# Optimization experiments

Measured on AMD Instinct MI355X. Metric: run time of the kernel, lower is better.

Reference implementation:

```python
import jax, jax.numpy as jnp
import numpy as np

D_MODEL = 1024
NUM_HEADS = 16
D_HEAD = D_MODEL // NUM_HEADS
THETA = 10000.0
B, S = 2, 2048


def setup_inputs() -> dict:
    key = jax.random.key(0)
    ks = jax.random.split(key, 5)
    std = np.sqrt(2.0 / (D_MODEL + D_MODEL))
    x = jax.random.normal(ks[0], (B, S, D_MODEL), dtype=jnp.float32)
    Wq = jax.random.normal(ks[1], (D_MODEL, D_MODEL), dtype=jnp.float32) * std
    Wk = jax.random.normal(ks[2], (D_MODEL, D_MODEL), dtype=jnp.float32) * std
    Wv = jax.random.normal(ks[3], (D_MODEL, D_MODEL), dtype=jnp.float32) * std
    Wo = jax.random.normal(ks[4], (D_MODEL, D_MODEL), dtype=jnp.float32) * std
    token_positions = jnp.arange(S, dtype=jnp.int32)
    return {"x": x, "Wq": Wq, "Wk": Wk, "Wv": Wv, "Wo": Wo,
            "token_positions": token_positions}


def _apply_rope(t, token_positions):
    # t: [B, H, S, d_head]; interleaved (even/odd) RoPE
    dh = t.shape[-1]
    inv_freq = 1.0 / (THETA ** (jnp.arange(0, dh, 2, dtype=jnp.float32) / dh))
    freqs = token_positions.astype(jnp.float32)[:, None] * inv_freq  # [S, dh/2]
    cos = jnp.cos(freqs)  # broadcasts over B, H
    sin = jnp.sin(freqs)
    x1 = t[..., 0::2]
    x2 = t[..., 1::2]
    r1 = x1 * cos - x2 * sin
    r2 = x1 * sin + x2 * cos
    return jnp.stack([r1, r2], axis=-1).reshape(t.shape)


def reference(x, Wq, Wk, Wv, Wo, token_positions):
    b, s, d = x.shape
    h, dh = NUM_HEADS, D_HEAD

    def proj(W):
        y = x @ W.T  # [B, S, D]
        return y.reshape(b, s, h, dh).transpose(0, 2, 1, 3)  # [B, H, S, dh]

    q = _apply_rope(proj(Wq), token_positions)
    k = _apply_rope(proj(Wk), token_positions)
    v = proj(Wv)

    scores = jnp.einsum('bhqd,bhkd->bhqk', q, k) / jnp.sqrt(jnp.float32(dh))
    causal = jnp.tril(jnp.ones((s, s), dtype=bool))
    scores = jnp.where(causal, scores, jnp.float32(-jnp.inf))
    attn = jax.nn.softmax(scores, axis=-1)
    out = jnp.einsum('bhqk,bhkd->bhqd', attn, v)  # [B, H, S, dh]
    out = out.transpose(0, 2, 1, 3).reshape(b, s, d)
    return out @ Wo.T
```

## Files before the change

### kernel.cpp

```cpp
#include <hip/hip_runtime.h>
#include <hip/hip_bf16.h>
#include <math.h>

#define DMODEL 1024
#define NHEAD  16
#define DHEAD  64
#define BATCH  2
#define SEQ    2048
#define MROWS  (BATCH * SEQ)

typedef __attribute__((ext_vector_type(8))) __bf16 bf16x8;
typedef __attribute__((ext_vector_type(4))) float  f32x4;

__device__ __forceinline__ void load16_lds(const ushort* g, ushort* l) {
    __builtin_amdgcn_global_load_lds(
        (const __attribute__((address_space(1))) unsigned int*)g,
        (__attribute__((address_space(3))) unsigned int*)l, 16, 0, 0);
}

__device__ __forceinline__ ushort bf16u(float v) {
    __hip_bfloat16 h = __float2bfloat16(v);
    return *reinterpret_cast<ushort*>(&h);
}

__global__ __launch_bounds__(256)
void cast_f32_bf16(const float* __restrict__ s, ushort* __restrict__ d, int n) {
    const int i = (blockIdx.x * 256 + threadIdx.x) * 8;
    if (i >= n) return;
    const f32x4 a = *reinterpret_cast<const f32x4*>(s + i);
    const f32x4 b = *reinterpret_cast<const f32x4*>(s + i + 4);
    bf16x8 o;
    #pragma unroll
    for (int j = 0; j < 4; j++) { o[j] = (__bf16)a[j]; o[4 + j] = (__bf16)b[j]; }
    *reinterpret_cast<bf16x8*>(d + i) = o;
}

__global__ __launch_bounds__(256)
void cast_w4(const float* __restrict__ w0, const float* __restrict__ w1,
             const float* __restrict__ w2, const float* __restrict__ w3,
             ushort* __restrict__ dst) {
    const float* src = (blockIdx.y == 0) ? w0 : (blockIdx.y == 1) ? w1
                     : (blockIdx.y == 2) ? w2 : w3;
    const int i = (blockIdx.x * 256 + threadIdx.x) * 8;
    const f32x4 a = *reinterpret_cast<const f32x4*>(src + i);
    const f32x4 b = *reinterpret_cast<const f32x4*>(src + i + 4);
    bf16x8 o;
    #pragma unroll
    for (int j = 0; j < 4; j++) { o[j] = (__bf16)a[j]; o[4 + j] = (__bf16)b[j]; }
    *reinterpret_cast<bf16x8*>(dst + (size_t)blockIdx.y * DMODEL * DMODEL + i) = o;
}

__global__ __launch_bounds__(256)
void gemm_qkv(const ushort* __restrict__ A, const ushort* __restrict__ B,
              ushort* __restrict__ C) {
    __shared__ __align__(16) ushort As[128 * 32];
    __shared__ __align__(16) ushort Bs[128 * 32];
    const int tid  = threadIdx.x;
    const int m0   = blockIdx.y * 128;
    const int n0   = blockIdx.x * 128;
    const int lane = tid & 63;
    const int w    = tid >> 6;
    const int l16  = lane & 15;
    const int quad = lane >> 4;
    const int wm   = (w >> 1) * 64;
    const int wn   = (w & 1) * 64;
    const int srow = tid >> 2;
    const int scol = (tid & 3) * 8;

    f32x4 acc[4][4];
    #pragma unroll
    for (int i = 0; i < 4; i++)
        #pragma unroll
        for (int j = 0; j < 4; j++) acc[i][j] = (f32x4){0.f, 0.f, 0.f, 0.f};

    for (int k0 = 0; k0 < DMODEL; k0 += 32) {
        __syncthreads();
        #pragma unroll
        for (int half = 0; half < 2; half++) {
            const int row = srow + half * 64;
            load16_lds(A + (size_t)(m0 + row) * DMODEL + k0 + scol,
                       &As[row * 32 + scol]);
            load16_lds(B + (size_t)(n0 + row) * DMODEL + k0 + scol,
                       &Bs[row * 32 + scol]);
        }
        __syncthreads();
        bf16x8 af[4], bfr[4];
        #pragma unroll
        for (int s = 0; s < 4; s++)
            af[s] = *reinterpret_cast<const bf16x8*>(
                &As[(wm + s * 16 + l16) * 32 + quad * 8]);
        #pragma unroll
        for (int s = 0; s < 4; s++)
            bfr[s] = *reinterpret_cast<const bf16x8*>(
                &Bs[(wn + s * 16 + l16) * 32 + quad * 8]);
        #pragma unroll
        for (int i = 0; i < 4; i++)
            #pragma unroll
            for (int j = 0; j < 4; j++)
                acc[i][j] = __builtin_amdgcn_mfma_f32_16x16x32_bf16(
                    af[i], bfr[j], acc[i][j], 0, 0, 0);
    }

    const int nbase  = n0 + wn;
    const int tensor = nbase >> 10;
    const int hh     = (nbase & 1023) >> 6;
    if (tensor < 2) {
        ushort* Dt = C + (size_t)tensor * ((size_t)MROWS * DMODEL);
        #pragma unroll
        for (int i = 0; i < 4; i++)
            #pragma unroll
            for (int r = 0; r < 4; r++) {
                const int m  = m0 + wm + i * 16 + quad * 4 + r;
                const int bb = m >> 11;
                const int ss = m & (SEQ - 1);
                #pragma unroll
                for (int j = 0; j < 4; j++) {
                    const int dh = j * 16 + l16;
                    Dt[(((size_t)(bb * NHEAD + hh)) * SEQ + ss) * DHEAD + dh] =
                        bf16u(acc[i][j][r]);
                }
            }
    } else {
        ushort* Dv = C + 2 * ((size_t)MROWS * DMODEL);
        #pragma unroll
        for (int i = 0; i < 4; i++)
            #pragma unroll
            for (int r = 0; r < 4; r++) {
                const int m = m0 + wm + i * 16 + quad * 4 + r;
                #pragma unroll
                for (int j = 0; j < 4; j++) {
                    const int row = hh * 64 + j * 16 + l16;
                    Dv[(size_t)row * MROWS + m] = bf16u(acc[i][j][r]);
                }
            }
    }
}

__global__ __launch_bounds__(256)
void gemm_out64(const ushort* __restrict__ A, const ushort* __restrict__ B,
                float* __restrict__ C) {
    __shared__ __align__(16) ushort As[64 * 32];
    __shared__ __align__(16) ushort Bs[128 * 32];
    const int tid  = threadIdx.x;
    const int m0   = blockIdx.y * 64;
    const int n0   = blockIdx.x * 128;
    const int lane = tid & 63;
    const int w    = tid >> 6;
    const int l16  = lane & 15;
    const int quad = lane >> 4;
    const int wm   = (w >> 1) * 32;
    const int wn   = (w & 1) * 64;
    const int srow = tid >> 2;
    const int scol = (tid & 3) * 8;

    f32x4 acc[2][4];
    #pragma unroll
    for (int i = 0; i < 2; i++)
        #pragma unroll
        for (int j = 0; j < 4; j++) acc[i][j] = (f32x4){0.f, 0.f, 0.f, 0.f};

    for (int k0 = 0; k0 < DMODEL; k0 += 32) {
        __syncthreads();
        {
            const int m  = m0 + srow;
            const int bb = m >> 11;
            const int ss = m & (SEQ - 1);
            const int kk = k0 + scol;
            const int h  = kk >> 6;
            const int dh = kk & 63;
            load16_lds(A + (((size_t)(bb * NHEAD + h)) * SEQ + ss) * DHEAD + dh,
                       &As[srow * 32 + scol]);
        }
        #pragma unroll
        for (int half = 0; half < 2; half++) {
            const int row = srow + half * 64;
            load16_lds(B + (size_t)(n0 + row) * DMODEL + k0 + scol,
                       &Bs[row * 32 + scol]);
        }
        __syncthreads();
        bf16x8 af[2], bfr[4];
        #pragma unroll
        for (int s = 0; s < 2; s++)
            af[s] = *reinterpret_cast<const bf16x8*>(
                &As[(wm + s * 16 + l16) * 32 + quad * 8]);
        #pragma unroll
        for (int s = 0; s < 4; s++)
            bfr[s] = *reinterpret_cast<const bf16x8*>(
                &Bs[(wn + s * 16 + l16) * 32 + quad * 8]);
        #pragma unroll
        for (int i = 0; i < 2; i++)
            #pragma unroll
            for (int j = 0; j < 4; j++)
                acc[i][j] = __builtin_amdgcn_mfma_f32_16x16x32_bf16(
                    af[i], bfr[j], acc[i][j], 0, 0, 0);
    }
    #pragma unroll
    for (int i = 0; i < 2; i++)
        #pragma unroll
        for (int r = 0; r < 4; r++) {
            const int m = m0 + wm + i * 16 + quad * 4 + r;
            #pragma unroll
            for (int j = 0; j < 4; j++)
                C[(size_t)m * DMODEL + n0 + wn + j * 16 + l16] = acc[i][j][r];
        }
}

__global__ __launch_bounds__(256)
void rope_bf16(__hip_bfloat16* __restrict__ q, __hip_bfloat16* __restrict__ k,
               const int* __restrict__ pos) {
    const int idx = blockIdx.x * blockDim.x + threadIdx.x;
    const int total = BATCH * NHEAD * SEQ * (DHEAD / 2);
    if (idx >= total) return;
    const int i  = idx & 31;
    const int s  = (idx >> 5) & (SEQ - 1);
    const int bh = idx >> 16;
    const float p = (float)pos[s];
    const float freq = p * powf(10000.0f, -(float)(2 * i) / (float)DHEAD);
    float sn, cs;
    sincosf(freq, &sn, &cs);
    const size_t base = (((size_t)bh * SEQ + s) * DHEAD) + 2 * i;
    float x1 = __bfloat162float(q[base]), x2 = __bfloat162float(q[base + 1]);
    q[base]     = __float2bfloat16(x1 * cs - x2 * sn);
    q[base + 1] = __float2bfloat16(x1 * sn + x2 * cs);
    x1 = __bfloat162float(k[base]); x2 = __bfloat162float(k[base + 1]);
    k[base]     = __float2bfloat16(x1 * cs - x2 * sn);
    k[base + 1] = __float2bfloat16(x1 * sn + x2 * cs);
}

__global__ __launch_bounds__(256)
void attn_mfma6(const ushort* __restrict__ qb, const ushort* __restrict__ kb,
                const ushort* __restrict__ vtg, ushort* __restrict__ ob) {
    __shared__ __align__(16) ushort Ks[2][4096];
    __shared__ __align__(16) ushort Vs[2][4096];
    __shared__ ushort Pb[4][16][72];

    const int bh   = blockIdx.x;
    const int b    = bh >> 4;
    const int h    = bh & 15;
    const int qt   = (gridDim.y - 1) - blockIdx.y;
    const int tid  = threadIdx.x;
    const int w    = tid >> 6;
    const int lane = tid & 63;
    const int l16  = lane & 15;
    const int quad = lane >> 4;
    const size_t base = (size_t)bh * SEQ * DHEAD;

    const int qlo = qt * 64 + w * 16;

    const float SC = 0.125f * 1.44269504088896f;
    bf16x8 qa[2];
    {
        const size_t qo = base + (size_t)(qlo + l16) * DHEAD + quad * 8;
        qa[0] = *reinterpret_cast<const bf16x8*>(qb + qo);
        qa[1] = *reinterpret_cast<const bf16x8*>(qb + qo + 32);
        #pragma unroll
        for (int j = 0; j < 8; j++) {
            qa[0][j] = (__bf16)(SC * (float)qa[0][j]);
            qa[1][j] = (__bf16)(SC * (float)qa[1][j]);
        }
    }

    f32x4 oacc[4];
    #pragma unroll
    for (int s = 0; s < 4; s++) oacc[s] = (f32x4){0.f, 0.f, 0.f, 0.f};
    float l_ = 0.f;

    const int c0 = tid,        r0 = c0 >> 3, g0 = (c0 & 7) ^ (r0 & 7);
    const int c1 = 256 + tid,  r1 = c1 >> 3, g1 = (c1 & 7) ^ (r1 & 7);
    const ushort* kg0 = kb + base + (size_t)r0 * DHEAD + g0 * 8;
    const ushort* kg1 = kb + base + (size_t)r1 * DHEAD + g1 * 8;
    const ushort* vg0 = vtg + (size_t)(h * DHEAD + r0) * MROWS + b * SEQ + g0 * 8;
    const ushort* vg1 = vtg + (size_t)(h * DHEAD + r1) * MROWS + b * SEQ + g1 * 8;

    int koff[2][4];
    #pragma unroll
    for (int half = 0; half < 2; half++)
        #pragma unroll
        for (int sub = 0; sub < 4; sub++)
            koff[half][sub] = (sub * 16 + l16) * 64 +
                              (((half * 4 + quad) ^ (l16 & 7)) * 8);

    load16_lds(kg0, &Ks[0][c0 * 8]);
    load16_lds(kg1, &Ks[0][c1 * 8]);
    load16_lds(vg0, &Vs[0][c0 * 8]);
    load16_lds(vg1, &Vs[0][c1 * 8]);

    const int T = qt + 1;
    for (int t = 0; t < T; t++) {
        const int bf = t & 1;
        __syncthreads();
        if (t + 1 < T) {
            const size_t ko = (size_t)(t + 1) * 64 * DHEAD;
            const int    vo = (t + 1) * 64;
            load16_lds(kg0 + ko, &Ks[bf ^ 1][c0 * 8]);
            load16_lds(kg1 + ko, &Ks[bf ^ 1][c1 * 8]);
            load16_lds(vg0 + vo, &Vs[bf ^ 1][c0 * 8]);
            load16_lds(vg1 + vo, &Vs[bf ^ 1][c1 * 8]);
        }

        const bool diag = (t == qt);
        const int nsub = diag ? (w + 1) : 4;
        const int nhv  = diag ? ((w >> 1) + 1) : 2;

        f32x4 sacc[4];
        #pragma unroll
        for (int s = 0; s < 4; s++) sacc[s] = (f32x4){0.f, 0.f, 0.f, 0.f};
        #pragma unroll
        for (int half = 0; half < 2; half++)
            #pragma unroll
            for (int sub = 0; sub < 4; sub++)
                if (sub < nsub) {
                    const bf16x8 kf = *reinterpret_cast<const bf16x8*>(
                        &Ks[bf][koff[half][sub]]);
                    sacc[sub] = __builtin_amdgcn_mfma_f32_16x16x32_bf16(
                        kf, qa[half], sacc[sub], 0, 0, 0);
                }

        float ev[4][4];
        if (diag) {
            const int thr = qlo + l16 - t * 64;
            #pragma unroll
            for (int sub = 0; sub < 4; sub++)
                #pragma unroll
                for (int r = 0; r < 4; r++) {
                    const float e = (sub * 16 + quad * 4 + r <= thr)
                                        ? exp2f(sacc[sub][r]) : 0.f;
                    ev[sub][r] = e;
                    l_ += e;
                }
        } else {
            #pragma unroll
            for (int sub = 0; sub < 4; sub++)
                #pragma unroll
                for (int r = 0; r < 4; r++) {
                    const float e = exp2f(sacc[sub][r]);
                    ev[sub][r] = e;
                    l_ += e;
                }
        }

        #pragma unroll
        for (int sub = 0; sub < 4; sub++) {
            ushort4 pk;
            pk.x = bf16u(ev[sub][0]); pk.y = bf16u(ev[sub][1]);
            pk.z = bf16u(ev[sub][2]); pk.w = bf16u(ev[sub][3]);
            *reinterpret_cast<ushort4*>(&Pb[w][l16][sub * 16 + quad * 4]) = pk;
        }
        bf16x8 pa[2];
        pa[0] = *reinterpret_cast<const bf16x8*>(&Pb[w][l16][quad * 8]);
        pa[1] = *reinterpret_cast<const bf16x8*>(&Pb[w][l16][32 + quad * 8]);

        #pragma unroll
        for (int hk = 0; hk < 2; hk++) {
            if (hk >= nhv) break;
            #pragma unroll
            for (int sf = 0; sf < 4; sf++) {
                const bf16x8 vf = *reinterpret_cast<const bf16x8*>(
                    &Vs[bf][koff[hk][sf]]);
                oacc[sf] = __builtin_amdgcn_mfma_f32_16x16x32_bf16(
                    pa[hk], vf, oacc[sf], 0, 0, 0);
            }
        }
    }

    l_ += __shfl_xor(l_, 16, 64);
    l_ += __shfl_xor(l_, 32, 64);
    float inv[4];
    #pragma unroll
    for (int r = 0; r < 4; r++) inv[r] = 1.f / __shfl(l_, quad * 4 + r, 64);
    #pragma unroll
    for (int sub = 0; sub < 4; sub++)
        #pragma unroll
        for (int r = 0; r < 4; r++) {
            const int q = qlo + quad * 4 + r;
            ob[base + (size_t)q * DHEAD + sub * 16 + l16] =
                bf16u(oacc[sub][r] * inv[r]);
        }
}

extern "C" void kernel_launch(void* const* d_in, const int* in_sizes, int n_in,
                              void* d_out, int out_size, void* d_ws, size_t ws_size,
                              hipStream_t stream) {
    const float* x  = (const float*)d_in[0];
    const float* Wq = (const float*)d_in[1];
    const float* Wk = (const float*)d_in[2];
    const float* Wv = (const float*)d_in[3];
    const float* Wo = (const float*)d_in[4];
    const int* pos = (const int*)d_in[5];

    const size_t TEN = (size_t)MROWS * DMODEL;
    const size_t WEL = (size_t)DMODEL * DMODEL;
    ushort* xb   = (ushort*)d_ws;
    ushort* Wqkv = xb + TEN;
    ushort* Wob  = Wqkv + 3 * WEL;
    ushort* qb   = Wob + WEL;
    ushort* kb   = qb + TEN;
    ushort* vtb  = kb + TEN;
    ushort* ob   = vtb + TEN;

    dim3 blk(256);
    cast_f32_bf16<<<TEN / (8 * 256), blk, 0, stream>>>(x, xb, (int)TEN);
    dim3 gcw(WEL / (8 * 256), 4);
    cast_w4<<<gcw, blk, 0, stream>>>(Wq, Wk, Wv, Wo, Wqkv);

    dim3 gqkv(3 * DMODEL / 128, MROWS / 128);
    gemm_qkv<<<gqkv, blk, 0, stream>>>(xb, Wqkv, qb);

    const int npairs = BATCH * NHEAD * SEQ * (DHEAD / 2);
    rope_bf16<<<(npairs + 255) / 256, blk, 0, stream>>>(
        (__hip_bfloat16*)qb, (__hip_bfloat16*)kb, pos);

    dim3 gattn(BATCH * NHEAD, SEQ / 64);
    attn_mfma6<<<gattn, blk, 0, stream>>>(qb, kb, vtb, ob);

    dim3 gout(DMODEL / 128, MROWS / 64);
    gemm_out64<<<gout, blk, 0, stream>>>(ob, Wob, (float*)d_out);
}
```

Before: 204.8 us.

## Fuse RoPE into QKV GEMM epilogue, double-buffer GEMMs, coalesce V-transpose stores

Removes the standalone RoPE kernel. A small sin/cos table is precomputed per position, and the rotation is applied in the QKV GEMM epilogue, with a lane shuffle fetching the even/odd partner value. Both GEMMs now double-buffer their LDS tiles, prefetching the next K slice before computing the current one, which drops one barrier per iteration. The transposed V output is staged through swizzled LDS so each lane writes 16-byte coalesced chunks instead of scattered 2-byte stores. The cost is more LDS per block, which may reduce occupancy.

```diff
diff --git a/kernel.cpp b/kernel.cpp
--- a/kernel.cpp
+++ b/kernel.cpp
@@ -51,10 +51,23 @@
 }
 
 __global__ __launch_bounds__(256)
+void rope_tab(const int* __restrict__ pos, float2* __restrict__ tab) {
+    const int idx = blockIdx.x * 256 + threadIdx.x;
+    const int s = idx >> 5;
+    const int i = idx & 31;
+    const float p = (float)pos[s];
+    const float inv = exp2f(-(float)i * 0.41524101186092f);
+    float sn, cs;
+    sincosf(p * inv, &sn, &cs);
+    tab[idx] = make_float2(cs, sn);
+}
+
+__global__ __launch_bounds__(256)
 void gemm_qkv(const ushort* __restrict__ A, const ushort* __restrict__ B,
-              ushort* __restrict__ C) {
-    __shared__ __align__(16) ushort As[128 * 32];
-    __shared__ __align__(16) ushort Bs[128 * 32];
+              ushort* __restrict__ C, const float2* __restrict__ tab) {
+    __shared__ __align__(16) ushort pool[16384];
+    ushort* As = pool;
+    ushort* Bs = pool + 8192;
     const int tid  = threadIdx.x;
     const int m0   = blockIdx.y * 128;
     const int n0   = blockIdx.x * 128;
@@ -73,26 +86,38 @@
         #pragma unroll
         for (int j = 0; j < 4; j++) acc[i][j] = (f32x4){0.f, 0.f, 0.f, 0.f};
 
-    for (int k0 = 0; k0 < DMODEL; k0 += 32) {
+    #pragma unroll
+    for (int half = 0; half < 2; half++) {
+        const int row = srow + half * 64;
+        load16_lds(A + (size_t)(m0 + row) * DMODEL + scol, &As[row * 32 + scol]);
+        load16_lds(B + (size_t)(n0 + row) * DMODEL + scol, &Bs[row * 32 + scol]);
+    }
+
+    for (int t = 0; t < 32; t++) {
+        const int bf = t & 1;
         __syncthreads();
-        #pragma unroll
-        for (int half = 0; half < 2; half++) {
-            const int row = srow + half * 64;
-            load16_lds(A + (size_t)(m0 + row) * DMODEL + k0 + scol,
-                       &As[row * 32 + scol]);
-            load16_lds(B + (size_t)(n0 + row) * DMODEL + k0 + scol,
-                       &Bs[row * 32 + scol]);
-        }
-        __syncthreads();
+        if (t + 1 < 32) {
+            const int k0 = (t + 1) * 32;
+            const int o  = (bf ^ 1) * 4096;
+            #pragma unroll
+            for (int half = 0; half < 2; half++) {
+                const int row = srow + half * 64;
+                load16_lds(A + (size_t)(m0 + row) * DMODEL + k0 + scol,
+                           &As[o + row * 32 + scol]);
+                load16_lds(B + (size_t)(n0 + row) * DMODEL + k0 + scol,
+                           &Bs[o + row * 32 + scol]);
+            }
+        }
+        const int o = bf * 4096;
         bf16x8 af[4], bfr[4];
         #pragma unroll
         for (int s = 0; s < 4; s++)
             af[s] = *reinterpret_cast<const bf16x8*>(
-                &As[(wm + s * 16 + l16) * 32 + quad * 8]);
+                &As[o + (wm + s * 16 + l16) * 32 + quad * 8]);
         #pragma unroll
         for (int s = 0; s < 4; s++)
             bfr[s] = *reinterpret_cast<const bf16x8*>(
-                &Bs[(wn + s * 16 + l16) * 32 + quad * 8]);
+                &Bs[o + (wn + s * 16 + l16) * 32 + quad * 8]);
         #pragma unroll
         for (int i = 0; i < 4; i++)
             #pragma unroll
@@ -113,34 +138,53 @@
                 const int m  = m0 + wm + i * 16 + quad * 4 + r;
                 const int bb = m >> 11;
                 const int ss = m & (SEQ - 1);
+                const float2* trow = tab + ss * 32;
                 #pragma unroll
                 for (int j = 0; j < 4; j++) {
-                    const int dh = j * 16 + l16;
-                    Dt[(((size_t)(bb * NHEAD + hh)) * SEQ + ss) * DHEAD + dh] =
-                        bf16u(acc[i][j][r]);
+                    const int f = j * 16 + l16;
+                    const float2 cs = trow[f >> 1];
+                    const float val = acc[i][j][r];
+                    const float prt = __shfl_xor(val, 1, 64);
+                    const float out = (f & 1) ? (prt * cs.y + val * cs.x)
+                                              : (val * cs.x - prt * cs.y);
+                    Dt[(((size_t)(bb * NHEAD + hh)) * SEQ + ss) * DHEAD + f] =
+                        bf16u(out);
                 }
             }
     } else {
-        ushort* Dv = C + 2 * ((size_t)MROWS * DMODEL);
+        __syncthreads();
+        ushort* Tw = pool + w * 4096;
         #pragma unroll
         for (int i = 0; i < 4; i++)
             #pragma unroll
-            for (int r = 0; r < 4; r++) {
-                const int m = m0 + wm + i * 16 + quad * 4 + r;
+            for (int j = 0; j < 4; j++) {
+                const int f = j * 16 + l16;
                 #pragma unroll
-                for (int j = 0; j < 4; j++) {
-                    const int row = hh * 64 + j * 16 + l16;
-                    Dv[(size_t)row * MROWS + m] = bf16u(acc[i][j][r]);
+                for (int r = 0; r < 4; r++) {
+                    const int ml = i * 16 + quad * 4 + r;
+                    Tw[f * 64 + (ml ^ ((f & 7) << 3))] = bf16u(acc[i][j][r]);
                 }
             }
+        ushort* Dv = C + 2 * ((size_t)MROWS * DMODEL);
+        const int c  = lane & 7;
+        const int fb = lane >> 3;
+        #pragma unroll
+        for (int rr = 0; rr < 8; rr++) {
+            const int fl = rr * 8 + fb;
+            const uint4 v = *reinterpret_cast<const uint4*>(
+                &Tw[fl * 64 + ((c << 3) ^ ((fl & 7) << 3))]);
+            *reinterpret_cast<uint4*>(
+                &Dv[(size_t)(hh * 64 + fl) * MROWS + m0 + wm + (c << 3)]) = v;
+        }
     }
 }
 
 __global__ __launch_bounds__(256)
 void gemm_out64(const ushort* __restrict__ A, const ushort* __restrict__ B,
                 float* __restrict__ C) {
-    __shared__ __align__(16) ushort As[64 * 32];
-    __shared__ __align__(16) ushort Bs[128 * 32];
+    __shared__ __align__(16) ushort pool[12288];
+    ushort* As = pool;
+    ushort* Bs = pool + 4096;
     const int tid  = threadIdx.x;
     const int m0   = blockIdx.y * 64;
     const int n0   = blockIdx.x * 128;
@@ -153,40 +197,53 @@
     const int srow = tid >> 2;
     const int scol = (tid & 3) * 8;
 
+    const int am  = m0 + srow;
+    const int abb = am >> 11;
+    const int ass = am & (SEQ - 1);
+    const size_t abase = ((size_t)(abb * NHEAD)) * SEQ * DHEAD + (size_t)ass * DHEAD;
+
     f32x4 acc[2][4];
     #pragma unroll
     for (int i = 0; i < 2; i++)
         #pragma unroll
         for (int j = 0; j < 4; j++) acc[i][j] = (f32x4){0.f, 0.f, 0.f, 0.f};
 
-    for (int k0 = 0; k0 < DMODEL; k0 += 32) {
-        __syncthreads();
-        {
-            const int m  = m0 + srow;
-            const int bb = m >> 11;
-            const int ss = m & (SEQ - 1);
-            const int kk = k0 + scol;
-            const int h  = kk >> 6;
-            const int dh = kk & 63;
-            load16_lds(A + (((size_t)(bb * NHEAD + h)) * SEQ + ss) * DHEAD + dh,
-                       &As[srow * 32 + scol]);
-        }
+    {
+        const int h = scol >> 6, dh = scol & 63;
+        load16_lds(A + abase + (size_t)h * SEQ * DHEAD + dh, &As[srow * 32 + scol]);
         #pragma unroll
         for (int half = 0; half < 2; half++) {
             const int row = srow + half * 64;
-            load16_lds(B + (size_t)(n0 + row) * DMODEL + k0 + scol,
-                       &Bs[row * 32 + scol]);
-        }
+            load16_lds(B + (size_t)(n0 + row) * DMODEL + scol, &Bs[row * 32 + scol]);
+        }
+    }
+
+    for (int t = 0; t < 32; t++) {
+        const int bf = t & 1;
         __syncthreads();
+        if (t + 1 < 32) {
+            const int k0 = (t + 1) * 32;
+            const int kk = k0 + scol;
+            const int h = kk >> 6, dh = kk & 63;
+            load16_lds(A + abase + (size_t)h * SEQ * DHEAD + dh,
+                       &As[(bf ^ 1) * 2048 + srow * 32 + scol]);
+            #pragma unroll
+            for (int half = 0; half < 2; half++) {
+                const int row = srow + half * 64;
+                load16_lds(B + (size_t)(n0 + row) * DMODEL + k0 + scol,
+                           &Bs[(bf ^ 1) * 4096 + row * 32 + scol]);
+            }
+        }
+        const int oa = bf * 2048, ob_ = bf * 4096;
         bf16x8 af[2], bfr[4];
         #pragma unroll
         for (int s = 0; s < 2; s++)
             af[s] = *reinterpret_cast<const bf16x8*>(
-                &As[(wm + s * 16 + l16) * 32 + quad * 8]);
+                &As[oa + (wm + s * 16 + l16) * 32 + quad * 8]);
         #pragma unroll
         for (int s = 0; s < 4; s++)
             bfr[s] = *reinterpret_cast<const bf16x8*>(
-                &Bs[(wn + s * 16 + l16) * 32 + quad * 8]);
+                &Bs[ob_ + (wn + s * 16 + l16) * 32 + quad * 8]);
         #pragma unroll
         for (int i = 0; i < 2; i++)
             #pragma unroll
@@ -203,28 +260,6 @@
             for (int j = 0; j < 4; j++)
                 C[(size_t)m * DMODEL + n0 + wn + j * 16 + l16] = acc[i][j][r];
         }
-}
-
-__global__ __launch_bounds__(256)
-void rope_bf16(__hip_bfloat16* __restrict__ q, __hip_bfloat16* __restrict__ k,
-               const int* __restrict__ pos) {
-    const int idx = blockIdx.x * blockDim.x + threadIdx.x;
-    const int total = BATCH * NHEAD * SEQ * (DHEAD / 2);
-    if (idx >= total) return;
-    const int i  = idx & 31;
-    const int s  = (idx >> 5) & (SEQ - 1);
-    const int bh = idx >> 16;
-    const float p = (float)pos[s];
-    const float freq = p * powf(10000.0f, -(float)(2 * i) / (float)DHEAD);
-    float sn, cs;
-    sincosf(freq, &sn, &cs);
-    const size_t base = (((size_t)bh * SEQ + s) * DHEAD) + 2 * i;
-    float x1 = __bfloat162float(q[base]), x2 = __bfloat162float(q[base + 1]);
-    q[base]     = __float2bfloat16(x1 * cs - x2 * sn);
-    q[base + 1] = __float2bfloat16(x1 * sn + x2 * cs);
-    x1 = __bfloat162float(k[base]); x2 = __bfloat162float(k[base + 1]);
-    k[base]     = __float2bfloat16(x1 * cs - x2 * sn);
-    k[base + 1] = __float2bfloat16(x1 * sn + x2 * cs);
 }
 
 __global__ __launch_bounds__(256)
@@ -397,18 +432,16 @@
     ushort* kb   = qb + TEN;
     ushort* vtb  = kb + TEN;
     ushort* ob   = vtb + TEN;
+    float2* tab  = (float2*)(ob + TEN);
 
     dim3 blk(256);
+    rope_tab<<<(SEQ * 32) / 256, blk, 0, stream>>>(pos, tab);
     cast_f32_bf16<<<TEN / (8 * 256), blk, 0, stream>>>(x, xb, (int)TEN);
     dim3 gcw(WEL / (8 * 256), 4);
     cast_w4<<<gcw, blk, 0, stream>>>(Wq, Wk, Wv, Wo, Wqkv);
 
     dim3 gqkv(3 * DMODEL / 128, MROWS / 128);
-    gemm_qkv<<<gqkv, blk, 0, stream>>>(xb, Wqkv, qb);
-
-    const int npairs = BATCH * NHEAD * SEQ * (DHEAD / 2);
-    rope_bf16<<<(npairs + 255) / 256, blk, 0, stream>>>(
-        (__hip_bfloat16*)qb, (__hip_bfloat16*)kb, pos);
+    gemm_qkv<<<gqkv, blk, 0, stream>>>(xb, Wqkv, qb, tab);
 
     dim3 gattn(BATCH * NHEAD, SEQ / 64);
     attn_mfma6<<<gattn, blk, 0, stream>>>(qb, kb, vtb, ob);
```

Measured after the change: 188.8 us. 7.8% less time.
